# Kernel optimization log

Hardware: AMD Instinct MI355X
Metric: run time of the kernel (lower is better)

## Reference

```python
import jax, jax.numpy as jnp
import numpy as np

B, S, D, H, E, KW = 2, 2048, 1024, 8, 128, 16  # batch, seq, d_model, heads, head_width, kernel_width


def setup_inputs() -> dict:
    key = jax.random.key(0)
    ks = jax.random.split(key, 10)
    sc = D ** -0.5
    x = jax.random.normal(ks[0], (B, S, D), dtype=jnp.float32)
    Wq = jax.random.normal(ks[1], (H, D, E), dtype=jnp.float32) * sc
    bq = jnp.zeros((H, E), dtype=jnp.float32)
    Wk = jax.random.normal(ks[2], (H, D, E), dtype=jnp.float32) * sc
    bk = jnp.zeros((H, E), dtype=jnp.float32)
    Wv = jax.random.normal(ks[3], (H, D, E), dtype=jnp.float32) * sc
    bv = jnp.zeros((H, E), dtype=jnp.float32)
    Wo = jax.random.normal(ks[4], (H, E, D), dtype=jnp.float32) * ((H * E) ** -0.5)
    bo = jnp.zeros((D,), dtype=jnp.float32)
    dilations = jnp.array([1, 1, 2, 2, 4, 4, 8, 8], dtype=jnp.int32)
    return {"x": x, "Wq": Wq, "bq": bq, "Wk": Wk, "bk": bk,
            "Wv": Wv, "bv": bv, "Wo": Wo, "bo": bo, "dilations": dilations}


def _windows(kh, vh, bkh, bvh, d):
    # kh, vh: [B, S, E] projected keys/values for one head; d: dilation (scalar int)
    s = kh.shape[1]
    # center-justified dilated window: positions i + d*j - d*(KW-1)//2
    pos = jnp.arange(s)[:, None] + d * jnp.arange(KW)[None, :] - (d * (KW - 1)) // 2
    valid = (pos >= 0) & (pos < s)            # [S, KW]
    posc = jnp.clip(pos, 0, s - 1)
    # padded positions hold the zero-embedding, whose projection is just the bias
    kw = jnp.where(valid[None, :, :, None], kh[:, posc, :], bkh)  # [B, S, KW, E]
    vw = jnp.where(valid[None, :, :, None], vh[:, posc, :], bvh)
    return kw, vw


def _lcsa(x, Wq, bq, Wk, bk, Wv, bv, Wo, bo, dilations):
    # per-head independent projections (Core.Linear with parallel shape [heads])
    q = jnp.einsum('bsd,hde->bhse', x, Wq) + bq[None, :, None, :]       # [B,H,S,E]
    k_all = jnp.einsum('bsd,hde->bhse', x, Wk) + bk[None, :, None, :]
    v_all = jnp.einsum('bsd,hde->bhse', x, Wv) + bv[None, :, None, :]
    # gather dilated local windows per head (project-then-gather; padded = bias)
    kw, vw = jax.vmap(_windows, in_axes=(1, 1, 0, 0, 0))(k_all, v_all, bk, bv, dilations)
    # kw, vw: [H, B, S, KW, E]
    logits = jnp.einsum('bhse,hbske->bhsk', q, kw)                       # [B,H,S,KW]
    score = jax.nn.softmax(logits, axis=-1)
    # NOTE: original divides by sqrt(d_head) AFTER softmax*value (faithful quirk)
    attn = jnp.einsum('bhsk,hbske->bhse', score, vw) / jnp.sqrt(jnp.asarray(E, x.dtype))
    out = jnp.einsum('bhse,hed->bsd', attn, Wo) + bo                     # dehead merge
    return out


def reference(x, Wq, bq, Wk, bk, Wv, bv, Wo, bo, dilations):
    return _lcsa(x, Wq, bq, Wk, bk, Wv, bv, Wo, bo, dilations)
```

## Files before the change

### kernel.cpp

```cpp
#include <hip/hip_runtime.h>
#include <stdint.h>

#define Bb 2
#define Ss 2048
#define Dd 1024
#define Hh 8
#define Ee 128
#define KWW 16
#define Mm (Bb*Ss)
#define Kk 1024

typedef unsigned short u16;
typedef __attribute__((ext_vector_type(8))) _Float16 f16x8;
typedef __attribute__((ext_vector_type(4))) float f32x4;

__device__ __forceinline__ u16 f2h(float f) {
  union { _Float16 h; u16 u; } v; v.h = (_Float16)f; return v.u;
}
__device__ __forceinline__ float h2f(u16 u) {
  union { u16 u; _Float16 h; } v; v.u = u; return (float)v.h;
}
__device__ __forceinline__ float h2f_lo(uint32_t w) { return h2f((u16)(w & 0xFFFF)); }
__device__ __forceinline__ float h2f_hi(uint32_t w) { return h2f((u16)(w >> 16)); }

__device__ __forceinline__ void gll16(const void* g, void* l) {
  __builtin_amdgcn_global_load_lds((const __attribute__((address_space(1))) void*)g,
                                   (__attribute__((address_space(3))) void*)l, 16, 0, 0);
}

__global__ __launch_bounds__(256) void prep(
    const float* __restrict__ x, const float* __restrict__ Wq,
    const float* __restrict__ Wk, const float* __restrict__ Wv,
    const float* __restrict__ Wo,
    u16* __restrict__ xh, u16* __restrict__ wT, u16* __restrict__ woT) {
  const int bid = blockIdx.x;
  const int tid = threadIdx.x;
  if (bid < 4096) {
    int i = (bid * 256 + tid) * 4;
    float4 f = *(const float4*)(x + i);
    uint64_t pk = (uint64_t)f2h(f.x) | ((uint64_t)f2h(f.y) << 16) |
                  ((uint64_t)f2h(f.z) << 32) | ((uint64_t)f2h(f.w) << 48);
    *(uint64_t*)(xh + i) = pk;
    return;
  }
  __shared__ float tile[32][33];
  const int tx = tid & 31, ty = tid >> 5;
  if (bid < 4096 + 3072) {
    const int idx = bid - 4096;
    const int z = idx >> 7, rem = idx & 127;
    const int h = z & 7;
    const float* W = (z < 8) ? Wq : (z < 16) ? Wk : Wv;
    const float* ib = W + (size_t)h * Dd * Ee;
    u16* ob = wT + (size_t)z * Ee * Kk;
    const int r0 = (rem & 31) * 32, c0 = (rem >> 5) * 32;
    #pragma unroll
    for (int kq = 0; kq < 4; kq++)
      tile[ty + 8*kq][tx] = ib[(size_t)(r0 + ty + 8*kq) * Ee + (c0 + tx)];
    __syncthreads();
    const int k = r0 + tx;
    #pragma unroll
    for (int kq = 0; kq < 4; kq++) {
      const int n = c0 + ty + 8*kq;
      ob[(((size_t)(k >> 3) * 128 + n) << 3) + (k & 7)] = f2h(tile[tx][ty + 8*kq]);
    }
  } else {
    const int idx = bid - (4096 + 3072);
    const int r0 = (idx & 31) * 32, c0 = (idx >> 5) * 32;
    const int C = Dd;
    #pragma unroll
    for (int kq = 0; kq < 4; kq++)
      tile[ty + 8*kq][tx] = Wo[(size_t)(r0 + ty + 8*kq) * C + (c0 + tx)];
    __syncthreads();
    const int k = r0 + tx;
    #pragma unroll
    for (int kq = 0; kq < 4; kq++) {
      const int n = c0 + ty + 8*kq;
      woT[(size_t)(n >> 7) * 131072 +
          (((size_t)(k >> 3) * 128 + (n & 127)) << 3) + (k & 7)] = f2h(tile[tx][ty + 8*kq]);
    }
  }
}

template<int MT>
__device__ __forceinline__ void gemm_core(
    const u16* __restrict__ A, const u16* __restrict__ Btf,
    u16* As, f32x4 (&acc)[MT / 32][4]) {
  constexpr int MI = MT / 32;
  const int tid = threadIdx.x;
  const int wave = tid >> 6;
  const int lane = tid & 63;
  const size_t lnoff = (size_t)(lane >> 3) * Kk + (size_t)(((lane & 7) ^ (lane >> 3)) * 8);

  const int wm = (wave >> 1) * (MT / 2);
  const int wn = (wave & 1) * 64;
  const int fr = lane & 15;
  const int q  = lane >> 4;
  const int sw = fr & 7;

  const u16* bptr = Btf + ((size_t)q * 128 + wn + fr) * 8;
  f16x8 bcur[8], bnxt[8];
  #pragma unroll
  for (int ks = 0; ks < 2; ks++)
    #pragma unroll
    for (int j = 0; j < 4; j++)
      bcur[ks * 4 + j] = *(const f16x8*)(bptr + (ks * 4) * 1024 + j * 128);

  #pragma unroll
  for (int i = 0; i < MI; i++)
    #pragma unroll
    for (int j = 0; j < 4; j++)
      #pragma unroll
      for (int r = 0; r < 4; r++) acc[i][j][r] = 0.0f;

  #pragma unroll
  for (int c = 0; c < MI; c++)
    gll16(A + lnoff + (size_t)((c * 4 + wave) * 8) * Kk, As + (c * 4 + wave) * 512);
  __syncthreads();

  for (int w = 0; w < Kk / 64; w++) {
    const int kt = w * 64;
    u16* cur = As + (w & 1) * (MT * 64);
    u16* nxt = As + ((w + 1) & 1) * (MT * 64);
    if (w + 1 < Kk / 64) {
      #pragma unroll
      for (int c = 0; c < MI; c++)
        gll16(A + lnoff + (size_t)((c * 4 + wave) * 8) * Kk + kt + 64, nxt + (c * 4 + wave) * 512);
    }
    const int ktn = (kt + 64) & (Kk - 1);
    #pragma unroll
    for (int ks = 0; ks < 2; ks++)
      #pragma unroll
      for (int j = 0; j < 4; j++)
        bnxt[ks * 4 + j] = *(const f16x8*)(bptr + ((ktn >> 3) + ks * 4) * 1024 + j * 128);
    #pragma unroll
    for (int ks = 0; ks < 2; ks++) {
      const int col = ((ks << 2) | q) ^ sw;
      f16x8 ah[MI];
      #pragma unroll
      for (int i = 0; i < MI; i++)
        ah[i] = *(const f16x8*)(cur + (wm + i * 16 + fr) * 64 + col * 8);
      #pragma unroll
      for (int i = 0; i < MI; i++)
        #pragma unroll
        for (int j = 0; j < 4; j++)
          acc[i][j] = __builtin_amdgcn_mfma_f32_16x16x32_f16(ah[i], bcur[ks * 4 + j], acc[i][j], 0, 0, 0);
    }
    __syncthreads();
    #pragma unroll
    for (int t = 0; t < 8; t++) bcur[t] = bnxt[t];
  }
}


__global__ __launch_bounds__(256) void gemm_qkv(
    const u16* __restrict__ xh, const u16* __restrict__ wT,
    const float* __restrict__ bq, const float* __restrict__ bk, const float* __restrict__ bv,
    u16* __restrict__ q, u16* __restrict__ k, u16* __restrict__ v) {
  __shared__ u16 As[128 * 64 * 2];
  const int wg = blockIdx.x;
  const int xcd = wg & 7;
  const int local = wg >> 3;
  const int m_l = local & 7;
  const int z_l = local >> 3;
  const int m0 = (((xcd & 3) * 8) + m_l) * 128;
  const int z = (xcd >> 2) * 12 + z_l;
  const int proj = z >> 3, h = z & 7;
  f32x4 acc[4][4];
  gemm_core<128>(xh + (size_t)m0 * Kk, wT + (size_t)z * (Ee * Kk), As, acc);

  u16* dst = proj == 0 ? q : (proj == 1 ? k : v);
  const float* bias = proj == 0 ? bq : (proj == 1 ? bk : bv);
  const int wave = threadIdx.x >> 6, lane = threadIdx.x & 63;
  const int wm = (wave >> 1) * 64, wn = (wave & 1) * 64;
  const int cn = lane & 15, rq4 = (lane >> 4) * 4;
  #pragma unroll
  for (int j = 0; j < 4; j++) {
    const int e = wn + j * 16 + cn;
    const float bb = bias[h * Ee + e];
    #pragma unroll
    for (int i = 0; i < 4; i++) {
      #pragma unroll
      for (int r = 0; r < 4; r++) {
        const int m = m0 + wm + i * 16 + rq4 + r;
        const int b = m >> 11, s = m & (Ss - 1);
        dst[(((size_t)(b * Hh + h)) * Ss + s) * Ee + e] = f2h(acc[i][j][r] + bb);
      }
    }
  }
}

__global__ __launch_bounds__(256) void gemm_out(
    const u16* __restrict__ attn, const u16* __restrict__ woT,
    const float* __restrict__ bo, float* __restrict__ out) {
  __shared__ u16 As[128 * 64 * 2];
  const int m0 = blockIdx.x * 128;
  const int n0 = blockIdx.y * 128;
  f32x4 acc[4][4];
  gemm_core<128>(attn + (size_t)m0 * Kk, woT + (size_t)blockIdx.y * 131072, As, acc);
  const int wave = threadIdx.x >> 6, lane = threadIdx.x & 63;
  const int wm = (wave >> 1) * 64, wn = (wave & 1) * 64;
  const int cn = lane & 15, rq4 = (lane >> 4) * 4;
  #pragma unroll
  for (int j = 0; j < 4; j++) {
    const int n = n0 + wn + j * 16 + cn;
    const float bb = bo[n];
    #pragma unroll
    for (int i = 0; i < 4; i++) {
      #pragma unroll
      for (int r = 0; r < 4; r++) {
        const int m = m0 + wm + i * 16 + rq4 + r;
        out[(size_t)m * Dd + n] = acc[i][j][r] + bb;
      }
    }
  }
}

__global__ __launch_bounds__(256) void attn_kernel(
    const u16* __restrict__ q, const u16* __restrict__ k, const u16* __restrict__ v,
    const float* __restrict__ bk, const float* __restrict__ bv,
    const int* __restrict__ dil, u16* __restrict__ attn) {
  const int nblk = (Bb * Hh * Ss) / 16;
  const int blk = (blockIdx.x & 7) * (nblk / 8) + (blockIdx.x >> 3);
  const int wid = blk * 4 + (threadIdx.x >> 6);
  const int lane = threadIdx.x & 63;
  const int grp = lane >> 4;
  const int lx = lane & 15;
  const int idx = wid * 4 + grp;
  const int s = idx & (Ss - 1);
  const int bh = idx >> 11;
  const int h = bh & 7, b = bh >> 3;
  const int d = dil[h];
  const size_t base = (size_t)bh * Ss * Ee;
  const u16* kp = k + base;
  const u16* vp = v + base;
  const int e0 = lx * 8;
  const int off = (d * (KWW - 1)) >> 1;

  float qf[8];
  {
    uint4 qw = *(const uint4*)(q + base + (size_t)s * Ee + e0);
    qf[0] = h2f_lo(qw.x); qf[1] = h2f_hi(qw.x);
    qf[2] = h2f_lo(qw.y); qf[3] = h2f_hi(qw.y);
    qf[4] = h2f_lo(qw.z); qf[5] = h2f_hi(qw.z);
    qf[6] = h2f_lo(qw.w); qf[7] = h2f_hi(qw.w);
  }
  float bkf[8], bvf[8];
  {
    const float4 a0 = ((const float4*)(bk + h * Ee + e0))[0];
    const float4 a1 = ((const float4*)(bk + h * Ee + e0))[1];
    bkf[0]=a0.x; bkf[1]=a0.y; bkf[2]=a0.z; bkf[3]=a0.w;
    bkf[4]=a1.x; bkf[5]=a1.y; bkf[6]=a1.z; bkf[7]=a1.w;
    const float4 c0 = ((const float4*)(bv + h * Ee + e0))[0];
    const float4 c1 = ((const float4*)(bv + h * Ee + e0))[1];
    bvf[0]=c0.x; bvf[1]=c0.y; bvf[2]=c0.z; bvf[3]=c0.w;
    bvf[4]=c1.x; bvf[5]=c1.y; bvf[6]=c1.z; bvf[7]=c1.w;
  }
  float blog = 0.f;
  #pragma unroll
  for (int i = 0; i < 8; i++) blog += qf[i] * bkf[i];
  uint4 bvh;
  bvh.x = (uint32_t)f2h(bvf[0]) | ((uint32_t)f2h(bvf[1]) << 16);
  bvh.y = (uint32_t)f2h(bvf[2]) | ((uint32_t)f2h(bvf[3]) << 16);
  bvh.z = (uint32_t)f2h(bvf[4]) | ((uint32_t)f2h(bvf[5]) << 16);
  bvh.w = (uint32_t)f2h(bvf[6]) | ((uint32_t)f2h(bvf[7]) << 16);

  float logit[KWW];
  #pragma unroll
  for (int j = 0; j < KWW; j++) {
    const int pos = s + d * j - off;
    const int posc = min(max(pos, 0), Ss - 1);
    uint4 kw = *(const uint4*)(kp + (size_t)posc * Ee + e0);
    float t = qf[0] * h2f_lo(kw.x) + qf[1] * h2f_hi(kw.x)
            + qf[2] * h2f_lo(kw.y) + qf[3] * h2f_hi(kw.y)
            + qf[4] * h2f_lo(kw.z) + qf[5] * h2f_hi(kw.z)
            + qf[6] * h2f_lo(kw.w) + qf[7] * h2f_hi(kw.w);
    logit[j] = (pos >= 0 && pos < Ss) ? t : blog;
  }

  uint4 vrow[KWW];
  #pragma unroll
  for (int j = 0; j < KWW; j++) {
    const int pos = s + d * j - off;
    const int posc = min(max(pos, 0), Ss - 1);
    uint4 vw = *(const uint4*)(vp + (size_t)posc * Ee + e0);
    const bool ok = (pos >= 0) && (pos < Ss);
    vrow[j].x = ok ? vw.x : bvh.x;
    vrow[j].y = ok ? vw.y : bvh.y;
    vrow[j].z = ok ? vw.z : bvh.z;
    vrow[j].w = ok ? vw.w : bvh.w;
  }

  {
    const bool hi = (lx & 8) != 0;
    #pragma unroll
    for (int jj = 0; jj < 8; jj++) {
      float send = hi ? logit[jj] : logit[jj + 8];
      float recv = __shfl_xor(send, 8, 64);
      logit[jj] = (hi ? logit[jj + 8] : logit[jj]) + recv;
    }
  }
  {
    const bool hi = (lx & 4) != 0;
    #pragma unroll
    for (int jj = 0; jj < 4; jj++) {
      float send = hi ? logit[jj] : logit[jj + 4];
      float recv = __shfl_xor(send, 4, 64);
      logit[jj] = (hi ? logit[jj + 4] : logit[jj]) + recv;
    }
  }
  {
    const bool hi = (lx & 2) != 0;
    #pragma unroll
    for (int jj = 0; jj < 2; jj++) {
      float send = hi ? logit[jj] : logit[jj + 2];
      float recv = __shfl_xor(send, 2, 64);
      logit[jj] = (hi ? logit[jj + 2] : logit[jj]) + recv;
    }
  }
  float own;
  {
    const bool hi = (lx & 1) != 0;
    float send = hi ? logit[0] : logit[1];
    float recv = __shfl_xor(send, 1, 64);
    own = (hi ? logit[1] : logit[0]) + recv;
  }

  float mx = own;
  mx = fmaxf(mx, __shfl_xor(mx, 1, 64));
  mx = fmaxf(mx, __shfl_xor(mx, 2, 64));
  mx = fmaxf(mx, __shfl_xor(mx, 4, 64));
  mx = fmaxf(mx, __shfl_xor(mx, 8, 64));
  float w = __expf(own - mx);
  float sum = w;
  sum += __shfl_xor(sum, 1, 64);
  sum += __shfl_xor(sum, 2, 64);
  sum += __shfl_xor(sum, 4, 64);
  sum += __shfl_xor(sum, 8, 64);
  w *= 1.0f / (sum * 11.313708498984760f);

  const int gbase = lane & 48;
  float gj[KWW];
  #pragma unroll
  for (int j = 0; j < KWW; j++)
    gj[j] = __shfl(w, gbase | j, 64);

  float acc[8];
  #pragma unroll
  for (int i = 0; i < 8; i++) acc[i] = 0.f;
  #pragma unroll
  for (int j = 0; j < KWW; j++) {
    const float wt = gj[j];
    acc[0] += wt * h2f_lo(vrow[j].x);
    acc[1] += wt * h2f_hi(vrow[j].x);
    acc[2] += wt * h2f_lo(vrow[j].y);
    acc[3] += wt * h2f_hi(vrow[j].y);
    acc[4] += wt * h2f_lo(vrow[j].z);
    acc[5] += wt * h2f_hi(vrow[j].z);
    acc[6] += wt * h2f_lo(vrow[j].w);
    acc[7] += wt * h2f_hi(vrow[j].w);
  }

  uint4 o;
  o.x = (uint32_t)f2h(acc[0]) | ((uint32_t)f2h(acc[1]) << 16);
  o.y = (uint32_t)f2h(acc[2]) | ((uint32_t)f2h(acc[3]) << 16);
  o.z = (uint32_t)f2h(acc[4]) | ((uint32_t)f2h(acc[5]) << 16);
  o.w = (uint32_t)f2h(acc[6]) | ((uint32_t)f2h(acc[7]) << 16);
  *(uint4*)(attn + (size_t)(b * Ss + s) * (Hh * Ee) + h * Ee + e0) = o;
}

extern "C" void kernel_launch(void* const* d_in, const int* in_sizes, int n_in,
                              void* d_out, int out_size, void* d_ws, size_t ws_size,
                              hipStream_t stream) {
  (void)in_sizes; (void)n_in; (void)out_size; (void)ws_size;
  const float* x  = (const float*)d_in[0];
  const float* Wq = (const float*)d_in[1];
  const float* bq = (const float*)d_in[2];
  const float* Wk = (const float*)d_in[3];
  const float* bk = (const float*)d_in[4];
  const float* Wv = (const float*)d_in[5];
  const float* bv = (const float*)d_in[6];
  const float* Wo = (const float*)d_in[7];
  const float* bo = (const float*)d_in[8];
  const int* dil  = (const int*)d_in[9];
  float* out = (float*)d_out;

  char* ws = (char*)d_ws;
  u16* xh  = (u16*)ws;  ws += (size_t)Mm * Kk * 2;
  u16* wT  = (u16*)ws;  ws += (size_t)24 * Ee * Kk * 2;
  u16* woT = (u16*)ws;  ws += (size_t)Kk * Dd * 2;
  u16* q = (u16*)ws; ws += (size_t)Bb * Hh * Ss * Ee * 2;
  u16* k = (u16*)ws; ws += (size_t)Bb * Hh * Ss * Ee * 2;
  u16* v = (u16*)ws; ws += (size_t)Bb * Hh * Ss * Ee * 2;
  u16* attn = xh;

  prep<<<8192, 256, 0, stream>>>(x, Wq, Wk, Wv, Wo, xh, wT, woT);
  gemm_qkv<<<768, 256, 0, stream>>>(xh, wT, bq, bk, bv, q, k, v);
  attn_kernel<<<(Bb * Hh * Ss) / 16, 256, 0, stream>>>(q, k, v, bk, bv, dil, attn);
  gemm_out<<<dim3(Mm / 128, Dd / 128), 256, 0, stream>>>(attn, woT, bo, out);
}
```

Baseline: 162.3 us.

## Pre-pack activations into MFMA fragment layout and drop LDS staging in GEMMs

The x conversion and the attention output now write fp16 data straight into a k-blocked fragment layout that matches what the MFMA operands expect. With that layout the GEMM inner loop loads A and B fragments directly from global memory into registers, so the LDS double buffer, global_load_lds and barriers are gone. The output GEMM also moves to 64-row tiles with 32 columns per wave, which doubles its block count. In exchange the GEMMs rely on L2/L1 reuse instead of shared-memory reuse, and the loads are no longer explicitly software-pipelined.

```diff
diff --git a/kernel.cpp b/kernel.cpp
--- a/kernel.cpp
+++ b/kernel.cpp
@@ -23,30 +23,34 @@
 __device__ __forceinline__ float h2f_lo(uint32_t w) { return h2f((u16)(w & 0xFFFF)); }
 __device__ __forceinline__ float h2f_hi(uint32_t w) { return h2f((u16)(w >> 16)); }
 
-__device__ __forceinline__ void gll16(const void* g, void* l) {
-  __builtin_amdgcn_global_load_lds((const __attribute__((address_space(1))) void*)g,
-                                   (__attribute__((address_space(3))) void*)l, 16, 0, 0);
-}
 
 __global__ __launch_bounds__(256) void prep(
     const float* __restrict__ x, const float* __restrict__ Wq,
     const float* __restrict__ Wk, const float* __restrict__ Wv,
     const float* __restrict__ Wo,
-    u16* __restrict__ xh, u16* __restrict__ wT, u16* __restrict__ woT) {
+    u16* __restrict__ xf, u16* __restrict__ wT, u16* __restrict__ woT) {
   const int bid = blockIdx.x;
   const int tid = threadIdx.x;
-  if (bid < 4096) {
-    int i = (bid * 256 + tid) * 4;
-    float4 f = *(const float4*)(x + i);
-    uint64_t pk = (uint64_t)f2h(f.x) | ((uint64_t)f2h(f.y) << 16) |
-                  ((uint64_t)f2h(f.z) << 32) | ((uint64_t)f2h(f.w) << 48);
-    *(uint64_t*)(xh + i) = pk;
+  if (bid < 2048) {
+    const int m0 = (bid >> 5) * 64, d0 = (bid & 31) * 32;
+    const int ml = tid & 63, dg = tid >> 6;
+    const int m = m0 + ml;
+    const float* src = x + (size_t)m * Dd + d0 + dg * 8;
+    float4 f0 = ((const float4*)src)[0];
+    float4 f1 = ((const float4*)src)[1];
+    uint4 o;
+    o.x = (uint32_t)f2h(f0.x) | ((uint32_t)f2h(f0.y) << 16);
+    o.y = (uint32_t)f2h(f0.z) | ((uint32_t)f2h(f0.w) << 16);
+    o.z = (uint32_t)f2h(f1.x) | ((uint32_t)f2h(f1.y) << 16);
+    o.w = (uint32_t)f2h(f1.z) | ((uint32_t)f2h(f1.w) << 16);
+    *(uint4*)(xf + ((size_t)(m >> 7) << 17) + (size_t)((d0 >> 3) + dg) * 1024 +
+              (size_t)(m & 127) * 8) = o;
     return;
   }
   __shared__ float tile[32][33];
   const int tx = tid & 31, ty = tid >> 5;
-  if (bid < 4096 + 3072) {
-    const int idx = bid - 4096;
+  if (bid < 2048 + 3072) {
+    const int idx = bid - 2048;
     const int z = idx >> 7, rem = idx & 127;
     const int h = z & 7;
     const float* W = (z < 8) ? Wq : (z < 16) ? Wk : Wv;
@@ -64,7 +68,7 @@
       ob[(((size_t)(k >> 3) * 128 + n) << 3) + (k & 7)] = f2h(tile[tx][ty + 8*kq]);
     }
   } else {
-    const int idx = bid - (4096 + 3072);
+    const int idx = bid - (2048 + 3072);
     const int r0 = (idx & 31) * 32, c0 = (idx >> 5) * 32;
     const int C = Dd;
     #pragma unroll
@@ -81,107 +85,70 @@
   }
 }
 
-template<int MT>
-__device__ __forceinline__ void gemm_core(
-    const u16* __restrict__ A, const u16* __restrict__ Btf,
-    u16* As, f32x4 (&acc)[MT / 32][4]) {
-  constexpr int MI = MT / 32;
-  const int tid = threadIdx.x;
-  const int wave = tid >> 6;
-  const int lane = tid & 63;
-  const size_t lnoff = (size_t)(lane >> 3) * Kk + (size_t)(((lane & 7) ^ (lane >> 3)) * 8);
-
-  const int wm = (wave >> 1) * (MT / 2);
-  const int wn = (wave & 1) * 64;
-  const int fr = lane & 15;
-  const int q  = lane >> 4;
-  const int sw = fr & 7;
-
-  const u16* bptr = Btf + ((size_t)q * 128 + wn + fr) * 8;
-  f16x8 bcur[8], bnxt[8];
-  #pragma unroll
-  for (int ks = 0; ks < 2; ks++)
-    #pragma unroll
-    for (int j = 0; j < 4; j++)
-      bcur[ks * 4 + j] = *(const f16x8*)(bptr + (ks * 4) * 1024 + j * 128);
-
+template<int MI, int NI>
+__device__ __forceinline__ void wave_gemm(
+    const u16* __restrict__ Af, const u16* __restrict__ Bf,
+    int m0, int n0, f32x4 (&acc)[MI][NI]) {
+  const int lane = threadIdx.x & 63;
+  const int fr = lane & 15, q = lane >> 4;
+  const u16* ap = Af + ((size_t)(m0 >> 7) << 17) + (size_t)q * 1024 +
+                  (size_t)((m0 & 127) + fr) * 8;
+  const u16* bp = Bf + (size_t)q * 1024 + (size_t)(n0 + fr) * 8;
   #pragma unroll
   for (int i = 0; i < MI; i++)
     #pragma unroll
-    for (int j = 0; j < 4; j++)
+    for (int j = 0; j < NI; j++)
       #pragma unroll
-      for (int r = 0; r < 4; r++) acc[i][j][r] = 0.0f;
-
-  #pragma unroll
-  for (int c = 0; c < MI; c++)
-    gll16(A + lnoff + (size_t)((c * 4 + wave) * 8) * Kk, As + (c * 4 + wave) * 512);
-  __syncthreads();
-
-  for (int w = 0; w < Kk / 64; w++) {
-    const int kt = w * 64;
-    u16* cur = As + (w & 1) * (MT * 64);
-    u16* nxt = As + ((w + 1) & 1) * (MT * 64);
-    if (w + 1 < Kk / 64) {
+      for (int r = 0; r < 4; r++) acc[i][j][r] = 0.f;
+  #pragma unroll 4
+  for (int w = 0; w < Kk / 32; w++) {
+    f16x8 av[MI], bv[NI];
+    #pragma unroll
+    for (int i = 0; i < MI; i++)
+      av[i] = *(const f16x8*)(ap + (size_t)w * 4096 + i * 128);
+    #pragma unroll
+    for (int j = 0; j < NI; j++)
+      bv[j] = *(const f16x8*)(bp + (size_t)w * 4096 + j * 128);
+    #pragma unroll
+    for (int i = 0; i < MI; i++)
       #pragma unroll
-      for (int c = 0; c < MI; c++)
-        gll16(A + lnoff + (size_t)((c * 4 + wave) * 8) * Kk + kt + 64, nxt + (c * 4 + wave) * 512);
-    }
-    const int ktn = (kt + 64) & (Kk - 1);
-    #pragma unroll
-    for (int ks = 0; ks < 2; ks++)
-      #pragma unroll
-      for (int j = 0; j < 4; j++)
-        bnxt[ks * 4 + j] = *(const f16x8*)(bptr + ((ktn >> 3) + ks * 4) * 1024 + j * 128);
-    #pragma unroll
-    for (int ks = 0; ks < 2; ks++) {
-      const int col = ((ks << 2) | q) ^ sw;
-      f16x8 ah[MI];
-      #pragma unroll
-      for (int i = 0; i < MI; i++)
-        ah[i] = *(const f16x8*)(cur + (wm + i * 16 + fr) * 64 + col * 8);
-      #pragma unroll
-      for (int i = 0; i < MI; i++)
-        #pragma unroll
-        for (int j = 0; j < 4; j++)
-          acc[i][j] = __builtin_amdgcn_mfma_f32_16x16x32_f16(ah[i], bcur[ks * 4 + j], acc[i][j], 0, 0, 0);
-    }
-    __syncthreads();
-    #pragma unroll
-    for (int t = 0; t < 8; t++) bcur[t] = bnxt[t];
+      for (int j = 0; j < NI; j++)
+        acc[i][j] = __builtin_amdgcn_mfma_f32_16x16x32_f16(av[i], bv[j], acc[i][j], 0, 0, 0);
   }
 }
 
 
 __global__ __launch_bounds__(256) void gemm_qkv(
-    const u16* __restrict__ xh, const u16* __restrict__ wT,
+    const u16* __restrict__ xf, const u16* __restrict__ wT,
     const float* __restrict__ bq, const float* __restrict__ bk, const float* __restrict__ bv,
     u16* __restrict__ q, u16* __restrict__ k, u16* __restrict__ v) {
-  __shared__ u16 As[128 * 64 * 2];
   const int wg = blockIdx.x;
   const int xcd = wg & 7;
   const int local = wg >> 3;
   const int m_l = local & 7;
   const int z_l = local >> 3;
-  const int m0 = (((xcd & 3) * 8) + m_l) * 128;
+  const int m0b = (((xcd & 3) * 8) + m_l) * 128;
   const int z = (xcd >> 2) * 12 + z_l;
   const int proj = z >> 3, h = z & 7;
+  const int wv = threadIdx.x >> 6;
+  const int m0 = m0b + (wv >> 1) * 64;
+  const int n0 = (wv & 1) * 64;
   f32x4 acc[4][4];
-  gemm_core<128>(xh + (size_t)m0 * Kk, wT + (size_t)z * (Ee * Kk), As, acc);
+  wave_gemm<4, 4>(xf, wT + ((size_t)z << 17), m0, n0, acc);
 
   u16* dst = proj == 0 ? q : (proj == 1 ? k : v);
   const float* bias = proj == 0 ? bq : (proj == 1 ? bk : bv);
-  const int wave = threadIdx.x >> 6, lane = threadIdx.x & 63;
-  const int wm = (wave >> 1) * 64, wn = (wave & 1) * 64;
+  const int lane = threadIdx.x & 63;
   const int cn = lane & 15, rq4 = (lane >> 4) * 4;
   #pragma unroll
   for (int j = 0; j < 4; j++) {
-    const int e = wn + j * 16 + cn;
+    const int e = n0 + j * 16 + cn;
     const float bb = bias[h * Ee + e];
     #pragma unroll
     for (int i = 0; i < 4; i++) {
       #pragma unroll
       for (int r = 0; r < 4; r++) {
-        const int m = m0 + wm + i * 16 + rq4 + r;
+        const int m = m0 + i * 16 + rq4 + r;
         const int b = m >> 11, s = m & (Ss - 1);
         dst[(((size_t)(b * Hh + h)) * Ss + s) * Ee + e] = f2h(acc[i][j][r] + bb);
       }
@@ -190,25 +157,26 @@
 }
 
 __global__ __launch_bounds__(256) void gemm_out(
-    const u16* __restrict__ attn, const u16* __restrict__ woT,
+    const u16* __restrict__ attnf, const u16* __restrict__ woT,
     const float* __restrict__ bo, float* __restrict__ out) {
-  __shared__ u16 As[128 * 64 * 2];
-  const int m0 = blockIdx.x * 128;
-  const int n0 = blockIdx.y * 128;
-  f32x4 acc[4][4];
-  gemm_core<128>(attn + (size_t)m0 * Kk, woT + (size_t)blockIdx.y * 131072, As, acc);
-  const int wave = threadIdx.x >> 6, lane = threadIdx.x & 63;
-  const int wm = (wave >> 1) * 64, wn = (wave & 1) * 64;
+  const int wv = threadIdx.x >> 6;
+  const int m0 = blockIdx.x * 64;
+  const int n0g = blockIdx.y * 128 + wv * 32;
+  const int nb = n0g >> 7;
+  const int n0 = n0g & 127;
+  f32x4 acc[4][2];
+  wave_gemm<4, 2>(attnf, woT + ((size_t)nb << 17), m0, n0, acc);
+  const int lane = threadIdx.x & 63;
   const int cn = lane & 15, rq4 = (lane >> 4) * 4;
   #pragma unroll
-  for (int j = 0; j < 4; j++) {
-    const int n = n0 + wn + j * 16 + cn;
+  for (int j = 0; j < 2; j++) {
+    const int n = n0g + j * 16 + cn;
     const float bb = bo[n];
     #pragma unroll
     for (int i = 0; i < 4; i++) {
       #pragma unroll
       for (int r = 0; r < 4; r++) {
-        const int m = m0 + wm + i * 16 + rq4 + r;
+        const int m = m0 + i * 16 + rq4 + r;
         out[(size_t)m * Dd + n] = acc[i][j][r] + bb;
       }
     }
@@ -218,7 +186,7 @@
 __global__ __launch_bounds__(256) void attn_kernel(
     const u16* __restrict__ q, const u16* __restrict__ k, const u16* __restrict__ v,
     const float* __restrict__ bk, const float* __restrict__ bv,
-    const int* __restrict__ dil, u16* __restrict__ attn) {
+    const int* __restrict__ dil, u16* __restrict__ attnf) {
   const int nblk = (Bb * Hh * Ss) / 16;
   const int blk = (blockIdx.x & 7) * (nblk / 8) + (blockIdx.x >> 3);
   const int wid = blk * 4 + (threadIdx.x >> 6);
@@ -365,7 +333,9 @@
   o.y = (uint32_t)f2h(acc[2]) | ((uint32_t)f2h(acc[3]) << 16);
   o.z = (uint32_t)f2h(acc[4]) | ((uint32_t)f2h(acc[5]) << 16);
   o.w = (uint32_t)f2h(acc[6]) | ((uint32_t)f2h(acc[7]) << 16);
-  *(uint4*)(attn + (size_t)(b * Ss + s) * (Hh * Ee) + h * Ee + e0) = o;
+  const int m = b * Ss + s;
+  *(uint4*)(attnf + ((size_t)(m >> 7) << 17) + (size_t)(h * 16 + lx) * 1024 +
+            (size_t)(m & 127) * 8) = o;
 }
 
 extern "C" void kernel_launch(void* const* d_in, const int* in_sizes, int n_in,
@@ -385,16 +355,16 @@
   float* out = (float*)d_out;
 
   char* ws = (char*)d_ws;
-  u16* xh  = (u16*)ws;  ws += (size_t)Mm * Kk * 2;
+  u16* xf  = (u16*)ws;  ws += (size_t)Mm * Kk * 2;
   u16* wT  = (u16*)ws;  ws += (size_t)24 * Ee * Kk * 2;
   u16* woT = (u16*)ws;  ws += (size_t)Kk * Dd * 2;
   u16* q = (u16*)ws; ws += (size_t)Bb * Hh * Ss * Ee * 2;
   u16* k = (u16*)ws; ws += (size_t)Bb * Hh * Ss * Ee * 2;
   u16* v = (u16*)ws; ws += (size_t)Bb * Hh * Ss * Ee * 2;
-  u16* attn = xh;
-
-  prep<<<8192, 256, 0, stream>>>(x, Wq, Wk, Wv, Wo, xh, wT, woT);
-  gemm_qkv<<<768, 256, 0, stream>>>(xh, wT, bq, bk, bv, q, k, v);
-  attn_kernel<<<(Bb * Hh * Ss) / 16, 256, 0, stream>>>(q, k, v, bk, bv, dil, attn);
-  gemm_out<<<dim3(Mm / 128, Dd / 128), 256, 0, stream>>>(attn, woT, bo, out);
-}
+  u16* attnf = xf;
+
+  prep<<<6144, 256, 0, stream>>>(x, Wq, Wk, Wv, Wo, xf, wT, woT);
+  gemm_qkv<<<768, 256, 0, stream>>>(xf, wT, bq, bk, bv, q, k, v);
+  attn_kernel<<<(Bb * Hh * Ss) / 16, 256, 0, stream>>>(q, k, v, bk, bv, dil, attnf);
+  gemm_out<<<dim3(Mm / 64, Dd / 128), 256, 0, stream>>>(attnf, woT, bo, out);
+}
```

Result: slower. 177.8 us (+9.5%).
